# Performance work log

Hardware: AMD Instinct MI355X
Metric: run time of the kernel (lower is better)

The kernel has to match this reference:

```python
import jax, jax.numpy as jnp
import numpy as np

TOTAL = 16384
IN_DIM = 512
OUT_DIM = 512
HEADS = 8
NUM_GRAPHS = 16


def setup_inputs() -> dict:
    key = jax.random.key(0)
    ks = jax.random.split(key, 8)
    x = jax.random.normal(ks[0], (TOTAL, IN_DIM), dtype=jnp.float32)
    batch = jnp.sort(jax.random.randint(ks[1], (TOTAL,), 0, NUM_GRAPHS)).astype(jnp.int64)
    s = 0.02
    # torch nn.MultiheadAttention packed in-projection: [3E, E] weight, [3E] bias
    in_proj_w = jax.random.normal(ks[2], (3 * IN_DIM, IN_DIM), dtype=jnp.float32) * s
    in_proj_b = jnp.zeros((3 * IN_DIM,), dtype=jnp.float32)
    out_proj_w = jax.random.normal(ks[3], (IN_DIM, IN_DIM), dtype=jnp.float32) * s
    out_proj_b = jnp.zeros((IN_DIM,), dtype=jnp.float32)
    lin_w = jax.random.normal(ks[4], (OUT_DIM, IN_DIM), dtype=jnp.float32) * s
    lin_b = jnp.zeros((OUT_DIM,), dtype=jnp.float32)
    return {"x": x, "batch": batch, "in_proj_w": in_proj_w, "in_proj_b": in_proj_b,
            "out_proj_w": out_proj_w, "out_proj_b": out_proj_b,
            "lin_w": lin_w, "lin_b": lin_b}


def _dense_indices(batch):
    """Host-side computation of (B, max_len, pos) from the sorted segment ids."""
    b_np = np.asarray(batch)
    B = int(b_np.max()) + 1
    counts = np.bincount(b_np, minlength=B)
    max_len = int(counts.max())
    offsets = np.concatenate([[0], np.cumsum(counts)[:-1]])  # start of each graph
    pos = jnp.asarray(np.arange(b_np.shape[0]) - offsets[b_np])  # within-graph index
    return B, max_len, pos


def reference(x, batch, in_proj_w, in_proj_b, out_proj_w, out_proj_b, lin_w, lin_b):
    T, E = x.shape
    H = HEADS
    D = E // H
    B, N, pos = _dense_indices(batch)

    # to_dense_batch: scatter ragged tokens into [B, N, E] + boolean mask [B, N]
    x_dense = jnp.zeros((B, N, E), x.dtype).at[batch, pos].set(x)
    mask = jnp.zeros((B, N), bool).at[batch, pos].set(True)

    # packed in-projection (torch MultiheadAttention semantics)
    qkv = x_dense @ in_proj_w.T + in_proj_b            # [B, N, 3E]
    q, k, v = jnp.split(qkv, 3, axis=-1)
    q = q.reshape(B, N, H, D)
    k = k.reshape(B, N, H, D)
    v = v.reshape(B, N, H, D)

    scores = jnp.einsum('bqhd,bkhd->bhqk', q, k) / jnp.sqrt(jnp.float32(D))
    # key_padding_mask = ~mask: padded keys are excluded
    scores = jnp.where(mask[:, None, None, :], scores, -jnp.inf)
    attn = jax.nn.softmax(scores, axis=-1)             # [B, H, N, N]
    ctx = jnp.einsum('bhqk,bkhd->bqhd', attn, v).reshape(B, N, E)
    attn_out = ctx @ out_proj_w.T + out_proj_b         # [B, N, E]

    y_dense = attn_out @ lin_w.T + lin_b               # [B, N, OUT_DIM]
    # unpad: x_out = y_dense[mask] == gather at the same (batch, pos) indices
    return y_dense[batch, pos]
```

## Files before the change

### kernel.cpp

```cpp
#include <hip/hip_runtime.h>
#include <stdint.h>
#include <stddef.h>

typedef unsigned short u16;
typedef unsigned int u32;
typedef __bf16 bf16x8 __attribute__((ext_vector_type(8)));
typedef _Float16 f16x8 __attribute__((ext_vector_type(8)));
typedef float f32x4 __attribute__((ext_vector_type(4)));

#define TT 16384
#define NG 16
#define MAXT 272
#define SCL 0.18033688011112042f

static __device__ __forceinline__ unsigned f2bf_u(float f) {
  unsigned u = __float_as_uint(f);
  return (u + 0x7fffu + ((u >> 16) & 1u)) >> 16;
}

static __device__ __forceinline__ void gl_lds16(const u16* g, u16* l) {
  __builtin_amdgcn_global_load_lds(
      (const __attribute__((address_space(1))) u32*)g,
      (__attribute__((address_space(3))) u32*)l, 16, 0, 0);
}

template <int CTRL>
static __device__ __forceinline__ float dppf(float x) {
  return __int_as_float(__builtin_amdgcn_mov_dpp(__float_as_int(x), CTRL, 0xF, 0xF, true));
}

#define NXF4 2097152
#define NWQ4 65536

__global__ __launch_bounds__(256) void cast_kernel(
    const float* __restrict__ x, const float* __restrict__ ipw,
    u16* __restrict__ xb, u16* __restrict__ ipwb) {
  const int base = blockIdx.x * 2048 + threadIdx.x;
#pragma unroll
  for (int u = 0; u < 8; ++u) {
    int j = base + u * 256;
    float4 f;
    if (j < NXF4) f = ((const float4*)x)[j];
    else          f = ((const float4*)ipw)[j - NXF4];
    if (j >= NXF4 && j < NXF4 + NWQ4) { f.x *= SCL; f.y *= SCL; f.z *= SCL; f.w *= SCL; }
    uint2 o;
    o.x = f2bf_u(f.x) | (f2bf_u(f.y) << 16);
    o.y = f2bf_u(f.z) | (f2bf_u(f.w) << 16);
    if (j < NXF4) ((uint2*)xb)[j] = o;
    else          ((uint2*)ipwb)[j - NXF4] = o;
  }
}

__global__ __launch_bounds__(256) void wc_seg_kernel(
    const int* __restrict__ batch, const float* __restrict__ ipb,
    float* __restrict__ bqk, int* __restrict__ seg,
    const float* __restrict__ Wl, const float* __restrict__ Wo,
    const float* __restrict__ bo, const float* __restrict__ bl,
    u16* __restrict__ Wc, float* __restrict__ bc) {
  const int tid = threadIdx.x;
  const int bxx = blockIdx.x;
  __shared__ float sWlT[512 * 20];
  __shared__ float red2[4096];
  __shared__ int scnt[NG];
  if (bxx < 256) {
    const int r0 = (bxx >> 3) << 4;
    const int c0 = (bxx & 7) << 6;
    for (int i = tid; i < 16 * 512; i += 256) {
      int r = i >> 9, k = i & 511;
      sWlT[k * 20 + r] = Wl[(r0 + r) * 512 + k];
    }
    __syncthreads();
    const int c = c0 + (tid & 63), ks = tid >> 6;
    float a[16];
#pragma unroll
    for (int r = 0; r < 16; ++r) a[r] = 0.f;
    const int kbeg = ks << 7;
#pragma unroll 4
    for (int kk = 0; kk < 128; ++kk) {
      int k = kbeg + kk;
      float w = Wo[k * 512 + c];
      const float4* sp = (const float4*)(sWlT + k * 20);
#pragma unroll
      for (int rq = 0; rq < 4; ++rq) {
        float4 v = sp[rq];
        a[rq * 4 + 0] += v.x * w; a[rq * 4 + 1] += v.y * w;
        a[rq * 4 + 2] += v.z * w; a[rq * 4 + 3] += v.w * w;
      }
    }
#pragma unroll
    for (int r = 0; r < 16; ++r) red2[(ks << 10) + (r << 6) + (tid & 63)] = a[r];
    __syncthreads();
#pragma unroll
    for (int q = 0; q < 4; ++q) {
      int oi = (q << 8) + tid;
      int r = oi >> 6, cc = oi & 63;
      float v = (red2[(r << 6) + cc] + red2[1024 + (r << 6) + cc]) +
                (red2[2048 + (r << 6) + cc] + red2[3072 + (r << 6) + cc]);
      Wc[(size_t)(r0 + r) * 512 + c0 + cc] = (u16)f2bf_u(v);
    }
    return;
  }
  if (bxx < 272) {
    const int row = ((bxx - 256) << 5) + (tid >> 3), s = tid & 7;
    float acc = 0.f;
#pragma unroll 8
    for (int j = 0; j < 64; ++j)
      acc += Wl[(size_t)row * 512 + (j << 3) + s] * bo[(j << 3) + s];
    acc += dppf<0xB1>(acc);
    acc += dppf<0x4E>(acc);
    acc += dppf<0x141>(acc);
    if (s == 0) bc[row] = acc + bl[row];
    return;
  }
  if (tid < NG) scnt[tid] = 0;
  __syncthreads();
  for (int i = tid; i < TT; i += 256) atomicAdd(&scnt[batch[i] & (NG - 1)], 1);
  for (int i = tid; i < 1024; i += 256) bqk[i] = ipb[i] * (i < 512 ? SCL : 1.f);
  __syncthreads();
  if (tid == 0) {
    int off = 0, nt = 0;
    for (int g = 0; g < NG; ++g) { seg[1 + g] = off; off += scnt[g]; }
    seg[1 + NG] = off;
    for (int g = 0; g < NG; ++g)
      for (int q0 = 0; q0 < scnt[g]; q0 += 64) { seg[32 + nt] = g; seg[320 + nt] = q0; ++nt; }
    seg[0] = nt;
  }
}

template <int EPI>
static __device__ __forceinline__ void gemm_core(
    u16* As, u16* Bs, int bidx,
    const u16* __restrict__ A, const u16* __restrict__ Bt, void* __restrict__ C,
    void* __restrict__ C2, const float* __restrict__ bias, int M, int N, int K) {
  const int nn = N >> 7;
  const int bm = bidx / nn, bn = bidx % nn;
  const int tid = threadIdx.x;
  const int w = tid >> 6, lane = tid & 63;
  const int quad = lane >> 4, l16 = lane & 15;
  const int wm = w >> 1, wn = w & 1;
  f32x4 acc[4][4];
#pragma unroll
  for (int mi = 0; mi < 4; ++mi)
#pragma unroll
    for (int ni = 0; ni < 4; ++ni) acc[mi][ni] = (f32x4){0.f, 0.f, 0.f, 0.f};
  const int sr = lane >> 3, scn = lane & 7;
  const int rowA0 = bm << 7, rowB0 = bn << 7;
  for (int kt = 0; kt < K; kt += 64) {
#pragma unroll
    for (int u = 0; u < 4; ++u) {
      int rbase = (w << 5) + (u << 3);
      int ml = rbase + sr;
      int ca = scn ^ (ml & 7);
      gl_lds16(A  + (size_t)(rowA0 + ml) * K + kt + ca * 8, As + (rbase << 6));
      gl_lds16(Bt + (size_t)(rowB0 + ml) * K + kt + ca * 8, Bs + (rbase << 6));
    }
    __syncthreads();
#pragma unroll
    for (int ks = 0; ks < 2; ++ks) {
      bf16x8 af[4], bfv[4];
#pragma unroll
      for (int mi = 0; mi < 4; ++mi) {
        int r = (wm << 6) + (mi << 4) + l16;
        af[mi] = *(const bf16x8*)(As + (r << 6) + ((((ks << 2) + quad) ^ (r & 7)) << 3));
      }
#pragma unroll
      for (int ni = 0; ni < 4; ++ni) {
        int r = (wn << 6) + (ni << 4) + l16;
        bfv[ni] = *(const bf16x8*)(Bs + (r << 6) + ((((ks << 2) + quad) ^ (r & 7)) << 3));
      }
#pragma unroll
      for (int mi = 0; mi < 4; ++mi)
#pragma unroll
        for (int ni = 0; ni < 4; ++ni)
          acc[mi][ni] = __builtin_amdgcn_mfma_f32_16x16x32_bf16(af[mi], bfv[ni], acc[mi][ni], 0, 0, 0);
    }
    __syncthreads();
  }
#pragma unroll
  for (int mi = 0; mi < 4; ++mi) {
#pragma unroll
    for (int ni = 0; ni < 4; ++ni) {
      int row = rowA0 + (wm << 6) + (mi << 4) + (quad << 2);
      int col = rowB0 + (wn << 6) + (ni << 4) + l16;
      float bvc = (EPI == 2) ? 0.f : bias[col];
#pragma unroll
      for (int r = 0; r < 4; ++r) {
        float v = acc[mi][ni][r] + ((EPI == 2) ? bias[row + r] : bvc);
        if (EPI == 0) {
          ((float*)C)[(size_t)(row + r) * N + col] = v;
        } else if (EPI == 1) {
          if (col < 512) {
            ((u16*)C)[(size_t)(row + r) * 512 + col] = (u16)f2bf_u(v);
          } else {
            int f = col - 512, hh = f >> 6, d = f & 63, t = row + r;
            ((u16*)C2)[(size_t)hh * (TT * 64) + ((t >> 6) << 12) + ((t & 63) << 6) + d] = (u16)f2bf_u(v);
          }
        } else {
          int f = row + r, hh = f >> 6, d = f & 63, t = col;
          ((u16*)C)[(size_t)hh * (TT * 64) + ((t >> 6) << 12) + (d << 6) + (t & 63)] =
              __builtin_bit_cast(unsigned short, (_Float16)v);
        }
      }
    }
  }
}

__global__ __launch_bounds__(256) void gemm_qkv(
    const u16* __restrict__ xb, const u16* __restrict__ ipwb,
    u16* __restrict__ qb, u16* __restrict__ kpk, u16* __restrict__ vpk,
    const float* __restrict__ bqk, const float* __restrict__ ipb) {
  __shared__ __align__(16) u16 As[128 * 64];
  __shared__ __align__(16) u16 Bs[128 * 64];
  if (blockIdx.x < 1024)
    gemm_core<1>(As, Bs, blockIdx.x, xb, ipwb, qb, kpk, bqk, TT, 1024, 512);
  else
    gemm_core<2>(As, Bs, blockIdx.x - 1024, ipwb + 1024 * 512, xb, vpk, nullptr,
                 ipb + 1024, 512, TT, 512);
}

__global__ __launch_bounds__(256) void gemm_out(
    const u16* __restrict__ ctxb, const u16* __restrict__ wcb,
    float* __restrict__ out, const float* __restrict__ bc) {
  __shared__ __align__(16) u16 As[128 * 64];
  __shared__ __align__(16) u16 Bs[128 * 64];
  gemm_core<0>(As, Bs, blockIdx.x, ctxb, wcb, out, nullptr, bc, TT, 512, 512);
}

__global__ __launch_bounds__(256, 4) void attn_kernel(
    const u16* __restrict__ qb, const u16* __restrict__ kpk,
    const u16* __restrict__ vpk, u16* __restrict__ ctx, const int* __restrict__ seg) {
  const int bx = blockIdx.x;
  if (bx >= seg[0]) return;
  const int h = blockIdx.y;
  const int g = seg[32 + bx], q0 = seg[320 + bx];
  const int s0 = seg[1 + g], len = seg[2 + g] - s0;
  const int tid = threadIdx.x, w = tid >> 6, lane = tid & 63;
  const int quad = lane >> 4, l16 = lane & 15;

  __shared__ __align__(16) u16 Ks[2][4096];
  __shared__ __align__(16) u16 Vs[2][4096];
  __shared__ __align__(16) u16 Ps[4096];

  const u16* kh = kpk + (size_t)h * (TT * 64);
  const u16* vh = vpk + (size_t)h * (TT * 64);

  bf16x8 afq[2];
#pragma unroll
  for (int ks = 0; ks < 2; ++ks) {
    int ql = (w << 4) + l16;
    uint4 tmp = {0u, 0u, 0u, 0u};
    if (q0 + ql < len)
      tmp = *(const uint4*)(qb + (size_t)(s0 + q0 + ql) * 512 + (h << 6) + (((ks << 2) + quad) << 3));
    afq[ks] = __builtin_bit_cast(bf16x8, tmp);
  }

  f32x4 lrow = (f32x4){0.f, 0.f, 0.f, 0.f};
  f32x4 O[4];
#pragma unroll
  for (int dt = 0; dt < 4; ++dt) O[dt] = (f32x4){0.f, 0.f, 0.f, 0.f};

  const int delta = s0 & 7;
  const int srl = lane >> 3, sc = lane & 7;
  int vcl = ((len - 8 + delta) & ~7) - delta;
  if (vcl < -delta) vcl = -delta;

  const int rb0 = (w << 4), rb1 = rb0 + 8;
  const int r0 = rb0 + srl, r1 = rb1 + srl;
  const int ca0 = sc ^ (r0 & 7), ca1 = sc ^ (r1 & 7);
  const int t0 = s0 - delta;
  int tk = t0 + r0;
  u32 kOffA = ((tk >> 6) << 12) + ((tk & 63) << 6) + (ca0 << 3);
  tk = t0 + r1;
  u32 kOffB = ((tk >> 6) << 12) + ((tk & 63) << 6) + (ca1 << 3);
  int tv = t0 + (ca0 << 3);
  u32 vOffA = ((tv >> 6) << 12) + (r0 << 6) + (tv & 63);
  tv = t0 + (ca1 << 3);
  u32 vOffB = ((tv >> 6) << 12) + (r1 << 6) + (tv & 63);

  auto stage = [&](int kv0, u16* bk, u16* bvs) {
    if (kv0 + 64 <= len) {
      gl_lds16(kh + kOffA, bk + (rb0 << 6));
      gl_lds16(kh + kOffB, bk + (rb1 << 6));
      gl_lds16(vh + vOffA, bvs + (rb0 << 6));
      gl_lds16(vh + vOffB, bvs + (rb1 << 6));
    } else {
      int tr = kv0 + r0; tr = tr < len - 1 ? tr : len - 1; int tc = s0 + tr;
      gl_lds16(kh + ((tc >> 6) << 12) + ((tc & 63) << 6) + (ca0 << 3), bk + (rb0 << 6));
      tr = kv0 + r1; tr = tr < len - 1 ? tr : len - 1; tc = s0 + tr;
      gl_lds16(kh + ((tc >> 6) << 12) + ((tc & 63) << 6) + (ca1 << 3), bk + (rb1 << 6));
      int st = kv0 + (ca0 << 3); st = st < len ? st : vcl; tc = s0 + st;
      gl_lds16(vh + ((tc >> 6) << 12) + (r0 << 6) + (tc & 63), bvs + (rb0 << 6));
      st = kv0 + (ca1 << 3); st = st < len ? st : vcl; tc = s0 + st;
      gl_lds16(vh + ((tc >> 6) << 12) + (r1 << 6) + (tc & 63), bvs + (rb1 << 6));
    }
    kOffA += 4096; kOffB += 4096; vOffA += 4096; vOffB += 4096;
  };

  const int nIt = (len + delta + 63) >> 6;
  u16* Pw = Ps + (w << 10);

  auto body = [&](int kv0, int i, const u16* Kc, const u16* Vc, u16* Kn, u16* Vn) {
    __syncthreads();
    if (i + 1 < nIt) stage(kv0 + 64, Kn, Vn);

    f32x4 s[4];
#pragma unroll
    for (int nt = 0; nt < 4; ++nt) s[nt] = (f32x4){0.f, 0.f, 0.f, 0.f};
    __builtin_amdgcn_s_setprio(1);
#pragma unroll
    for (int ks = 0; ks < 2; ++ks) {
#pragma unroll
      for (int nt = 0; nt < 4; ++nt) {
        int kr = (nt << 4) + l16;
        bf16x8 bk = *(const bf16x8*)(Kc + (kr << 6) + ((((ks << 2) + quad) ^ (kr & 7)) << 3));
        s[nt] = __builtin_amdgcn_mfma_f32_16x16x32_bf16(afq[ks], bk, s[nt], 0, 0, 0);
      }
    }
    __builtin_amdgcn_s_setprio(0);
    if ((kv0 < 0) | (kv0 + 64 > len)) {
#pragma unroll
      for (int nt = 0; nt < 4; ++nt) {
        int ki = kv0 + (nt << 4) + l16;
        float msk = ((unsigned)ki < (unsigned)len) ? 0.f : -1e30f;
#pragma unroll
        for (int r = 0; r < 4; ++r) s[nt][r] += msk;
      }
    }
#pragma unroll
    for (int nt = 0; nt < 4; ++nt)
#pragma unroll
      for (int r = 0; r < 4; ++r) s[nt][r] = __builtin_amdgcn_exp2f(s[nt][r]);
#pragma unroll
    for (int r = 0; r < 4; ++r)
      lrow[r] += (s[0][r] + s[1][r]) + (s[2][r] + s[3][r]);
#pragma unroll
    for (int nt = 0; nt < 4; ++nt)
#pragma unroll
      for (int r = 0; r < 4; ++r) {
        float a = s[nt][r];
        float b = dppf<0xB1>(a);
        if (!(l16 & 1)) {
          u32 p = __builtin_bit_cast(u32, __builtin_amdgcn_cvt_pkrtz(a, b));
          int prow = (quad << 2) + r, kc = (nt << 4) + l16;
          *(u32*)(Pw + (prow << 6) + (((kc >> 3) ^ (prow & 7)) << 3) + (kc & 7)) = p;
        }
      }
#pragma unroll
    for (int ks = 0; ks < 2; ++ks) {
      f16x8 ap = *(const f16x8*)(Pw + (l16 << 6) + ((((ks << 2) + quad) ^ (l16 & 7)) << 3));
      __builtin_amdgcn_s_setprio(1);
#pragma unroll
      for (int dt = 0; dt < 4; ++dt) {
        int vr = (dt << 4) + l16;
        f16x8 bv = *(const f16x8*)(Vc + (vr << 6) + ((((ks << 2) + quad) ^ (vr & 7)) << 3));
        O[dt] = __builtin_amdgcn_mfma_f32_16x16x32_f16(ap, bv, O[dt], 0, 0, 0);
      }
      __builtin_amdgcn_s_setprio(0);
    }
  };

  stage(-delta, Ks[0], Vs[0]);
  {
    int kv0 = -delta, i = 0;
    while (i < nIt) {
      body(kv0, i, Ks[0], Vs[0], Ks[1], Vs[1]);
      ++i; kv0 += 64;
      if (i >= nIt) break;
      body(kv0, i, Ks[1], Vs[1], Ks[0], Vs[0]);
      ++i; kv0 += 64;
    }
  }

  {
    f32x4 inv;
#pragma unroll
    for (int r = 0; r < 4; ++r) {
      float t = lrow[r];
      t += dppf<0xB1>(t);
      t += dppf<0x4E>(t);
      t += dppf<0x124>(t);
      t += dppf<0x128>(t);
      inv[r] = 1.f / t;
    }
#pragma unroll
    for (int dt = 0; dt < 4; ++dt)
#pragma unroll
      for (int r = 0; r < 4; ++r) {
        int ql = (w << 4) + (quad << 2) + r;
        if (q0 + ql < len)
          ctx[(size_t)(s0 + q0 + ql) * 512 + (h << 6) + (dt << 4) + l16] = (u16)f2bf_u(O[dt][r] * inv[r]);
      }
  }
}

extern "C" void kernel_launch(void* const* d_in, const int* in_sizes, int n_in,
                              void* d_out, int out_size, void* d_ws, size_t ws_size,
                              hipStream_t stream) {
  const float* x = (const float*)d_in[0];
  const int* batch = (const int*)d_in[1];
  const float* ipw = (const float*)d_in[2];
  const float* ipb = (const float*)d_in[3];
  const float* opw = (const float*)d_in[4];
  const float* opb = (const float*)d_in[5];
  const float* lw = (const float*)d_in[6];
  const float* lb = (const float*)d_in[7];
  float* out = (float*)d_out;
  char* ws = (char*)d_ws;

  u16* xb   = (u16*)(ws + 0);
  u16* ctxb = (u16*)(ws + 0);
  u16* qb   = (u16*)(ws + 16777216);
  u16* kpk  = (u16*)(ws + 33554432);
  u16* vpk  = (u16*)(ws + 50331648);
  u16* ipwb = (u16*)(ws + 67108864);
  u16* wcb  = (u16*)(ws + 68681728);
  float* bc = (float*)(ws + 69206016);
  float* bqk= (float*)(ws + 69208064);
  int* seg  = (int*)(ws + 69212160);

  cast_kernel<<<1120, 256, 0, stream>>>(x, ipw, xb, ipwb);
  wc_seg_kernel<<<273, 256, 0, stream>>>(batch, ipb, bqk, seg, lw, opw, opb, lb,
                                         wcb, bc);
  gemm_qkv<<<1536, 256, 0, stream>>>(xb, ipwb, qb, kpk, vpk, bqk, ipb);
  attn_kernel<<<dim3(MAXT, 8), 256, 0, stream>>>(qb, kpk, vpk, ctxb, seg);
  gemm_out<<<512, 256, 0, stream>>>(ctxb, wcb, out, bc);
  (void)in_sizes; (void)n_in; (void)out_size; (void)ws_size;
}
```

Measured before the change: 256.9 us.

## Keep attention probabilities in registers via swapped MFMA operands and permlane swaps

Swaps the A/B operands of the QK^T MFMA so each lane holds scores along the key dimension. The probabilities are then packed to f16 and rearranged with v_permlane16_swap into the A-operand layout of the PV MFMA, which removes the LDS round trip through the Ps buffer. The V read index is permuted to match, and the row-sum reduction is rebuilt with permlane swaps plus ds_bpermute. This cuts LDS traffic and shared memory use, at the cost of relying on subtle lane-layout correctness.

```diff
diff --git a/kernel.cpp b/kernel.cpp
--- a/kernel.cpp
+++ b/kernel.cpp
@@ -236,10 +236,10 @@
   const int s0 = seg[1 + g], len = seg[2 + g] - s0;
   const int tid = threadIdx.x, w = tid >> 6, lane = tid & 63;
   const int quad = lane >> 4, l16 = lane & 15;
+  const int qd = ((quad & 1) << 1) | (quad >> 1);
 
   __shared__ __align__(16) u16 Ks[2][4096];
   __shared__ __align__(16) u16 Vs[2][4096];
-  __shared__ __align__(16) u16 Ps[4096];
 
   const u16* kh = kpk + (size_t)h * (TT * 64);
   const u16* vh = vpk + (size_t)h * (TT * 64);
@@ -254,7 +254,7 @@
     afq[ks] = __builtin_bit_cast(bf16x8, tmp);
   }
 
-  f32x4 lrow = (f32x4){0.f, 0.f, 0.f, 0.f};
+  float lacc = 0.f;
   f32x4 O[4];
 #pragma unroll
   for (int dt = 0; dt < 4; ++dt) O[dt] = (f32x4){0.f, 0.f, 0.f, 0.f};
@@ -297,7 +297,6 @@
   };
 
   const int nIt = (len + delta + 63) >> 6;
-  u16* Pw = Ps + (w << 10);
 
   auto body = [&](int kv0, int i, const u16* Kc, const u16* Vc, u16* Kn, u16* Vn) {
     __syncthreads();
@@ -313,46 +312,46 @@
       for (int nt = 0; nt < 4; ++nt) {
         int kr = (nt << 4) + l16;
         bf16x8 bk = *(const bf16x8*)(Kc + (kr << 6) + ((((ks << 2) + quad) ^ (kr & 7)) << 3));
-        s[nt] = __builtin_amdgcn_mfma_f32_16x16x32_bf16(afq[ks], bk, s[nt], 0, 0, 0);
+        s[nt] = __builtin_amdgcn_mfma_f32_16x16x32_bf16(bk, afq[ks], s[nt], 0, 0, 0);
       }
     }
     __builtin_amdgcn_s_setprio(0);
     if ((kv0 < 0) | (kv0 + 64 > len)) {
 #pragma unroll
-      for (int nt = 0; nt < 4; ++nt) {
-        int ki = kv0 + (nt << 4) + l16;
-        float msk = ((unsigned)ki < (unsigned)len) ? 0.f : -1e30f;
-#pragma unroll
-        for (int r = 0; r < 4; ++r) s[nt][r] += msk;
-      }
+      for (int nt = 0; nt < 4; ++nt)
+#pragma unroll
+        for (int r = 0; r < 4; ++r) {
+          int ki = kv0 + (nt << 4) + (quad << 2) + r;
+          s[nt][r] += ((unsigned)ki < (unsigned)len) ? 0.f : -1e30f;
+        }
     }
 #pragma unroll
     for (int nt = 0; nt < 4; ++nt)
 #pragma unroll
       for (int r = 0; r < 4; ++r) s[nt][r] = __builtin_amdgcn_exp2f(s[nt][r]);
 #pragma unroll
-    for (int r = 0; r < 4; ++r)
-      lrow[r] += (s[0][r] + s[1][r]) + (s[2][r] + s[3][r]);
-#pragma unroll
     for (int nt = 0; nt < 4; ++nt)
-#pragma unroll
-      for (int r = 0; r < 4; ++r) {
-        float a = s[nt][r];
-        float b = dppf<0xB1>(a);
-        if (!(l16 & 1)) {
-          u32 p = __builtin_bit_cast(u32, __builtin_amdgcn_cvt_pkrtz(a, b));
-          int prow = (quad << 2) + r, kc = (nt << 4) + l16;
-          *(u32*)(Pw + (prow << 6) + (((kc >> 3) ^ (prow & 7)) << 3) + (kc & 7)) = p;
-        }
-      }
+      lacc += (s[nt][0] + s[nt][1]) + (s[nt][2] + s[nt][3]);
+
+    u32 pr[8];
+#pragma unroll
+    for (int nt = 0; nt < 4; ++nt) {
+      pr[nt * 2 + 0] = __builtin_bit_cast(u32, __builtin_amdgcn_cvt_pkrtz(s[nt][0], s[nt][1]));
+      pr[nt * 2 + 1] = __builtin_bit_cast(u32, __builtin_amdgcn_cvt_pkrtz(s[nt][2], s[nt][3]));
+    }
 #pragma unroll
     for (int ks = 0; ks < 2; ++ks) {
-      f16x8 ap = *(const f16x8*)(Pw + (l16 << 6) + ((((ks << 2) + quad) ^ (l16 & 7)) << 3));
+      u32 a0 = pr[4 * ks + 0], b0 = pr[4 * ks + 2];
+      u32 a1 = pr[4 * ks + 1], b1 = pr[4 * ks + 3];
+      asm("v_permlane16_swap_b32 %0, %1" : "+v"(a0), "+v"(b0));
+      asm("v_permlane16_swap_b32 %0, %1" : "+v"(a1), "+v"(b1));
+      uint4 apv = {a0, a1, b0, b1};
+      f16x8 ap = __builtin_bit_cast(f16x8, apv);
       __builtin_amdgcn_s_setprio(1);
 #pragma unroll
       for (int dt = 0; dt < 4; ++dt) {
         int vr = (dt << 4) + l16;
-        f16x8 bv = *(const f16x8*)(Vc + (vr << 6) + ((((ks << 2) + quad) ^ (vr & 7)) << 3));
+        f16x8 bv = *(const f16x8*)(Vc + (vr << 6) + ((((ks << 2) + qd) ^ (vr & 7)) << 3));
         O[dt] = __builtin_amdgcn_mfma_f32_16x16x32_f16(ap, bv, O[dt], 0, 0, 0);
       }
       __builtin_amdgcn_s_setprio(0);
@@ -372,15 +371,20 @@
   }
 
   {
+    u32 a = __float_as_uint(lacc), b = a;
+    asm("v_permlane32_swap_b32 %0, %1" : "+v"(a), "+v"(b));
+    float t = __uint_as_float(a) + __uint_as_float(b);
+    a = __float_as_uint(t); b = a;
+    asm("v_permlane16_swap_b32 %0, %1" : "+v"(a), "+v"(b));
+    lacc = __uint_as_float(a) + __uint_as_float(b);
+  }
+  {
     f32x4 inv;
 #pragma unroll
     for (int r = 0; r < 4; ++r) {
-      float t = lrow[r];
-      t += dppf<0xB1>(t);
-      t += dppf<0x4E>(t);
-      t += dppf<0x124>(t);
-      t += dppf<0x128>(t);
-      inv[r] = 1.f / t;
+      float Lr = __int_as_float(
+          __builtin_amdgcn_ds_bpermute((((quad << 2) + r) << 2), __float_as_int(lacc)));
+      inv[r] = 1.f / Lr;
     }
 #pragma unroll
     for (int dt = 0; dt < 4; ++dt)
```

New measurement: 241.5 us. 6.0% less time.
